# Optimization experiments

Measured on AMD Instinct MI355X. Metric: run time of the kernel, lower is better.

Reference implementation:

```python
import jax, jax.numpy as jnp
import numpy as np

B, D_IN, H, D_OUT = 4096, 4096, 2048, 1000
LN_EPS = 1e-5


def setup_inputs() -> dict:
    key = jax.random.key(0)
    ks = jax.random.split(key, 8)
    s_in = 1.0 / np.sqrt(H)  # torch RNN init: U(-1/sqrt(H), 1/sqrt(H))
    inp = {
        "x": jax.random.normal(ks[0], (B, D_IN), dtype=jnp.float32),
        "W_ih0": jax.random.uniform(ks[1], (H, D_IN), jnp.float32, -s_in, s_in),
        "b_ih0": jax.random.uniform(ks[2], (H,), jnp.float32, -s_in, s_in),
        "b_hh0": jax.random.uniform(ks[3], (H,), jnp.float32, -s_in, s_in),
        "W_ih1": jax.random.uniform(ks[4], (H, H), jnp.float32, -s_in, s_in),
        "b_ih1": jax.random.uniform(ks[5], (H,), jnp.float32, -s_in, s_in),
        "b_hh1": jax.random.uniform(ks[6], (H,), jnp.float32, -s_in, s_in),
        "ln_g": jnp.ones((2 * H,), jnp.float32),
        "ln_b": jnp.zeros((2 * H,), jnp.float32),
        "fc_W": jax.random.uniform(ks[7], (D_OUT, 2 * H), jnp.float32, -1.0 / np.sqrt(2 * H), 1.0 / np.sqrt(2 * H)),
        "fc_b": jnp.zeros((D_OUT,), jnp.float32),
    }
    return inp


def reference(x, W_ih0, b_ih0, b_hh0, W_ih1, b_ih1, b_hh1, ln_g, ln_b, fc_W, fc_b):
    # seq_len == 1, h0 == 0 -> W_hh terms vanish; only biases remain.
    h1 = jnp.tanh(x @ W_ih0.T + b_ih0 + b_hh0)          # [B, H]
    h2 = jnp.tanh(h1 @ W_ih1.T + b_ih1 + b_hh1)         # [B, H]
    # last_hidden == mean_pooled (single step) -> concat duplicates h2
    combined = jnp.concatenate([h2, h2], axis=1)        # [B, 2H]
    mu = combined.mean(axis=-1, keepdims=True)
    var = combined.var(axis=-1, keepdims=True)
    normed = (combined - mu) * jax.lax.rsqrt(var + LN_EPS) * ln_g + ln_b
    # dropout is identity in eval mode
    return normed @ fc_W.T + fc_b                        # [B, D_OUT]
```

## Files before the change

kernel.cpp:

```cpp
#include <hip/hip_runtime.h>
#include <hip/hip_bf16.h>

typedef __attribute__((ext_vector_type(8))) unsigned short ushort8;
typedef __attribute__((ext_vector_type(8))) __bf16 bf16x8;
typedef __attribute__((ext_vector_type(4))) float f32x4;
typedef __attribute__((ext_vector_type(4))) float floatx4;

__device__ __forceinline__ unsigned short f2bf(float f) {
    unsigned u = __builtin_bit_cast(unsigned, f);
    u += 0x7fffu + ((u >> 16) & 1u);
    return (unsigned short)(u >> 16);
}
__device__ __forceinline__ float bf2f(unsigned short h) {
    unsigned u = ((unsigned)h) << 16;
    return __builtin_bit_cast(float, u);
}

__device__ __forceinline__ void gload_lds16(const void* g, void* l) {
    __builtin_amdgcn_global_load_lds(
        (const __attribute__((address_space(1))) void*)g,
        (__attribute__((address_space(3))) void*)l,
        16, 0, 0);
}

#define BAR()   asm volatile("s_barrier" ::: "memory")
#define VMW0()  asm volatile("s_waitcnt vmcnt(0)" ::: "memory")

__global__ __launch_bounds__(256) void prep_kernel(
        const float* __restrict__ x,   unsigned short* __restrict__ xb,
        const float* __restrict__ W0,  unsigned short* __restrict__ w0b,
        const float* __restrict__ W1,  unsigned short* __restrict__ w1b,
        const float* __restrict__ fcW, const float* __restrict__ lng,
        const float* __restrict__ lnb, const float* __restrict__ fcb,
        unsigned short* __restrict__ weff, float* __restrict__ cc,
        float* __restrict__ wsum) {
    const int b = blockIdx.x;
    const int tid = threadIdx.x;
    __shared__ float red[4], redw[4];

    if (b < 14336) {
        const float* in; unsigned short* out; int i;
        if (b < 8192)       { in = x;  out = xb;  i = b * 256 + tid; }
        else if (b < 12288) { in = W0; out = w0b; i = (b - 8192) * 256 + tid; }
        else                { in = W1; out = w1b; i = (b - 12288) * 256 + tid; }
        floatx4 a = ((const floatx4*)in)[2 * i];
        floatx4 c = ((const floatx4*)in)[2 * i + 1];
        ushort8 o;
#pragma unroll
        for (int j = 0; j < 4; ++j) { o[j] = f2bf(a[j]); o[4 + j] = f2bf(c[j]); }
        ((ushort8*)out)[i] = o;
        return;
    }

    const int o = b - 14336;
    if (o >= 1000) {
        ushort8 z = {0, 0, 0, 0, 0, 0, 0, 0};
        ((ushort8*)(weff + (size_t)o * 2048))[tid] = z;
        if (tid == 0) { cc[o] = 0.f; wsum[o] = 0.f; }
        return;
    }
    const float* wrow = fcW + (size_t)o * 4096;
    int j0 = tid * 8;
    floatx4 wa  = *(const floatx4*)(wrow + j0);
    floatx4 wb  = *(const floatx4*)(wrow + j0 + 4);
    floatx4 wa2 = *(const floatx4*)(wrow + 2048 + j0);
    floatx4 wb2 = *(const floatx4*)(wrow + 2048 + j0 + 4);
    floatx4 ga  = *(const floatx4*)(lng + j0);
    floatx4 gb  = *(const floatx4*)(lng + j0 + 4);
    floatx4 ga2 = *(const floatx4*)(lng + 2048 + j0);
    floatx4 gb2 = *(const floatx4*)(lng + 2048 + j0 + 4);
    floatx4 ba  = *(const floatx4*)(lnb + j0);
    floatx4 bb  = *(const floatx4*)(lnb + j0 + 4);
    floatx4 ba2 = *(const floatx4*)(lnb + 2048 + j0);
    floatx4 bb2 = *(const floatx4*)(lnb + 2048 + j0 + 4);
    ushort8 o8;
    float acc = 0.f, ws = 0.f;
#pragma unroll
    for (int j = 0; j < 4; ++j) {
        o8[j] = f2bf(ga[j] * wa[j] + ga2[j] * wa2[j]);
        acc += ba[j] * wa[j] + ba2[j] * wa2[j];
        ws  += bf2f(o8[j]);
        o8[4 + j] = f2bf(gb[j] * wb[j] + gb2[j] * wb2[j]);
        acc += bb[j] * wb[j] + bb2[j] * wb2[j];
        ws  += bf2f(o8[4 + j]);
    }
    ((ushort8*)(weff + (size_t)o * 2048))[tid] = o8;
#pragma unroll
    for (int d = 32; d; d >>= 1) { acc += __shfl_down(acc, d); ws += __shfl_down(ws, d); }
    if ((tid & 63) == 0) { red[tid >> 6] = acc; redw[tid >> 6] = ws; }
    __syncthreads();
    if (tid == 0) {
        cc[o] = fcb[o] + red[0] + red[1] + red[2] + red[3];
        wsum[o] = redw[0] + redw[1] + redw[2] + redw[3];
    }
}

__global__ __launch_bounds__(256) void ln_stats(const unsigned short* __restrict__ h2,
                                                float2* __restrict__ mur) {
    int row = blockIdx.x, tid = threadIdx.x;
    ushort8 v = ((const ushort8*)(h2 + (size_t)row * 2048))[tid];
    float s = 0.f, s2 = 0.f;
#pragma unroll
    for (int j = 0; j < 8; ++j) { float f = bf2f(v[j]); s += f; s2 += f * f; }
#pragma unroll
    for (int d = 32; d; d >>= 1) { s += __shfl_down(s, d); s2 += __shfl_down(s2, d); }
    __shared__ float rs_[4], rs2_[4];
    if ((tid & 63) == 0) { rs_[tid >> 6] = s; rs2_[tid >> 6] = s2; }
    __syncthreads();
    if (tid == 0) {
        float S = rs_[0] + rs_[1] + rs_[2] + rs_[3];
        float S2 = rs2_[0] + rs2_[1] + rs2_[2] + rs2_[3];
        float mu = S * (1.f / 2048.f);
        float var = S2 * (1.f / 2048.f) - mu * mu;
        mur[row] = make_float2(mu, rsqrtf(var + 1e-5f));
    }
}

template <int EPI, int NJ>
__global__ __launch_bounds__(512, 2) void gemm_rp(const unsigned short* __restrict__ A,
                                                  const unsigned short* __restrict__ B,
                                                  int M, int N, int K,
                                                  const float* __restrict__ bias0,
                                                  const float* __restrict__ bias1,
                                                  void* __restrict__ Cout, int ncols,
                                                  const float2* __restrict__ mur,
                                                  const float* __restrict__ wsum) {
    extern __shared__ char smem[];
    constexpr int BUFSZ = 16384 + NJ * 8192;
    const int tid = threadIdx.x;
    const int lane = tid & 63, wid = tid >> 6;
    const int wm = wid >> 2, wn = wid & 3;
    const int fr = lane & 15, g = lane >> 4;

    const int nwg = gridDim.x * gridDim.y;
    const int fid = blockIdx.y * gridDim.x + blockIdx.x;
    const int cpx = nwg >> 3;
    const int sw = (fid & 7) * cpx + (fid >> 3);
    const int bx = sw % gridDim.x, by = sw / gridDim.x;
    const int row0 = by * 128, col0 = bx * (64 * NJ);

    const int tg = tid >> 3;
    const int tcE = ((tid & 7) ^ (tg & 7)) * 8;

    auto stage = [&](int kt, char* buf) {
#pragma unroll
        for (int r = 0; r < 2; ++r)
            gload_lds16(A + (size_t)(row0 + r * 64 + tg) * K + kt * 64 + tcE,
                        buf + r * 8192 + wid * 1024);
#pragma unroll
        for (int rr = 0; rr < NJ; ++rr)
            gload_lds16(B + (size_t)(col0 + rr * 64 + tg) * K + kt * 64 + tcE,
                        buf + 16384 + rr * 8192 + wid * 1024);
    };

    const int xorv = (fr & 7) << 4;
    auto readFrags = [&](bf16x8 (&fa)[4][2], bf16x8 (&fb)[NJ][2], const char* buf) {
#pragma unroll
        for (int m = 0; m < 4; ++m)
#pragma unroll
            for (int kh = 0; kh < 2; ++kh)
                fa[m][kh] = __builtin_bit_cast(bf16x8, *(const ushort8*)(
                    buf + (wm * 64 + m * 16 + fr) * 128 + ((kh * 64 + g * 16) ^ xorv)));
#pragma unroll
        for (int n = 0; n < NJ; ++n)
#pragma unroll
            for (int kh = 0; kh < 2; ++kh)
                fb[n][kh] = __builtin_bit_cast(bf16x8, *(const ushort8*)(
                    buf + 16384 + (wn * (16 * NJ) + n * 16 + fr) * 128 + ((kh * 64 + g * 16) ^ xorv)));
    };

    f32x4 acc[4][NJ];
#pragma unroll
    for (int i = 0; i < 4; ++i)
#pragma unroll
        for (int j = 0; j < NJ; ++j) acc[i][j] = f32x4{0.f, 0.f, 0.f, 0.f};

    auto domfma = [&](bf16x8 (&fa)[4][2], bf16x8 (&fb)[NJ][2]) {
        __builtin_amdgcn_s_setprio(1);
#pragma unroll
        for (int m = 0; m < 4; ++m)
#pragma unroll
            for (int n = 0; n < NJ; ++n)
#pragma unroll
                for (int kh = 0; kh < 2; ++kh)
                    acc[m][n] = __builtin_amdgcn_mfma_f32_16x16x32_bf16(fa[m][kh], fb[n][kh], acc[m][n], 0, 0, 0);
        __builtin_amdgcn_s_setprio(0);
    };

    bf16x8 aX[4][2], bX[NJ][2], aY[4][2], bY[NJ][2];

    stage(0, smem); stage(1, smem + BUFSZ);
    if constexpr (NJ == 4) { asm volatile("s_waitcnt vmcnt(6)" ::: "memory"); }
    else                   { asm volatile("s_waitcnt vmcnt(4)" ::: "memory"); }
    BAR();
    readFrags(aX, bX, smem);

    const int NT = K >> 6;
    for (int t = 0; t < NT; t += 2) {
        if (t + 2 < NT) {
            stage(t + 2, smem + ((t + 2) % 3) * BUFSZ);
            if constexpr (NJ == 4) { asm volatile("s_waitcnt vmcnt(6)" ::: "memory"); }
            else                   { asm volatile("s_waitcnt vmcnt(4)" ::: "memory"); }
        } else {
            VMW0();
        }
        BAR();
        readFrags(aY, bY, smem + ((t + 1) % 3) * BUFSZ);
        domfma(aX, bX);

        if (t + 2 < NT) {
            if (t + 3 < NT) {
                stage(t + 3, smem + ((t + 3) % 3) * BUFSZ);
                if constexpr (NJ == 4) { asm volatile("s_waitcnt vmcnt(6)" ::: "memory"); }
                else                   { asm volatile("s_waitcnt vmcnt(4)" ::: "memory"); }
            } else {
                VMW0();
            }
            BAR();
            readFrags(aX, bX, smem + ((t + 2) % 3) * BUFSZ);
        }
        domfma(aY, bY);
    }

#pragma unroll
    for (int i = 0; i < 4; ++i) {
        int rbase = row0 + wm * 64 + i * 16 + g * 4;
        if (EPI == 0) {
#pragma unroll
            for (int j = 0; j < NJ; ++j) {
                int col = col0 + wn * (16 * NJ) + j * 16 + fr;
                float bsum = bias0[col] + bias1[col];
                unsigned short* O = (unsigned short*)Cout;
#pragma unroll
                for (int r = 0; r < 4; ++r)
                    O[(size_t)(rbase + r) * N + col] = f2bf(tanhf(acc[i][j][r] + bsum));
            }
        } else {
            float2 mr[4];
#pragma unroll
            for (int r = 0; r < 4; ++r) mr[r] = mur[rbase + r];
#pragma unroll
            for (int j = 0; j < NJ; ++j) {
                int col = col0 + wn * (16 * NJ) + j * 16 + fr;
                if (col < ncols) {
                    float ws = wsum[col];
                    float ccv = bias0[col];
                    float* O = (float*)Cout;
#pragma unroll
                    for (int r = 0; r < 4; ++r)
                        O[(size_t)(rbase + r) * ncols + col] =
                            mr[r].y * (acc[i][j][r] - mr[r].x * ws) + ccv;
                }
            }
        }
    }
}

extern "C" void kernel_launch(void* const* d_in, const int* in_sizes, int n_in,
                              void* d_out, int out_size, void* d_ws, size_t ws_size,
                              hipStream_t stream) {
    const float* x   = (const float*)d_in[0];
    const float* W0  = (const float*)d_in[1];
    const float* bi0 = (const float*)d_in[2];
    const float* bh0 = (const float*)d_in[3];
    const float* W1  = (const float*)d_in[4];
    const float* bi1 = (const float*)d_in[5];
    const float* bh1 = (const float*)d_in[6];
    const float* lng = (const float*)d_in[7];
    const float* lnb = (const float*)d_in[8];
    const float* fcW = (const float*)d_in[9];
    const float* fcb = (const float*)d_in[10];
    float* out = (float*)d_out;

    char* w = (char*)d_ws;
    unsigned short* xb   = (unsigned short*)(w);
    unsigned short* w0b  = (unsigned short*)(w + 33554432ull);
    unsigned short* w1b  = (unsigned short*)(w + 50331648ull);
    unsigned short* h1   = (unsigned short*)(w + 58720256ull);
    unsigned short* h2   = (unsigned short*)(w + 75497472ull);
    unsigned short* weff = (unsigned short*)(w + 92274688ull);
    float* cc            = (float*)(w + 96468992ull);
    float* wsum          = (float*)(w + 96473088ull);
    float2* mur          = (float2*)(w + 96477184ull);

    const int SHM0 = 3 * (16384 + 4 * 8192);
    const int SHM1 = 3 * (16384 + 2 * 8192);
    (void)hipFuncSetAttribute((const void*)gemm_rp<0, 4>,
                              hipFuncAttributeMaxDynamicSharedMemorySize, SHM0);
    (void)hipFuncSetAttribute((const void*)gemm_rp<1, 2>,
                              hipFuncAttributeMaxDynamicSharedMemorySize, SHM1);

    prep_kernel<<<15360, 256, 0, stream>>>(x, xb, W0, w0b, W1, w1b,
                                           fcW, lng, lnb, fcb, weff, cc, wsum);
    gemm_rp<0, 4><<<dim3(8, 32), 512, SHM0, stream>>>(xb, w0b, 4096, 2048, 4096,
                                                      bi0, bh0, h1, 2048, nullptr, nullptr);
    gemm_rp<0, 4><<<dim3(8, 32), 512, SHM0, stream>>>(h1, w1b, 4096, 2048, 2048,
                                                      bi1, bh1, h2, 2048, nullptr, nullptr);
    ln_stats<<<4096, 256, 0, stream>>>(h2, mur);
    gemm_rp<1, 2><<<dim3(8, 32), 512, SHM1, stream>>>(h2, weff, 4096, 1024, 2048,
                                                      cc, nullptr, out, 1000, mur, wsum);
}
```

Baseline: 170.3 us.

## Fuse LayerNorm row statistics into second GEMM epilogue, drop ln_stats kernel

```diff
diff --git a/kernel.cpp b/kernel.cpp
--- a/kernel.cpp
+++ b/kernel.cpp
@@ -95,27 +95,6 @@
     }
 }
 
-__global__ __launch_bounds__(256) void ln_stats(const unsigned short* __restrict__ h2,
-                                                float2* __restrict__ mur) {
-    int row = blockIdx.x, tid = threadIdx.x;
-    ushort8 v = ((const ushort8*)(h2 + (size_t)row * 2048))[tid];
-    float s = 0.f, s2 = 0.f;
-#pragma unroll
-    for (int j = 0; j < 8; ++j) { float f = bf2f(v[j]); s += f; s2 += f * f; }
-#pragma unroll
-    for (int d = 32; d; d >>= 1) { s += __shfl_down(s, d); s2 += __shfl_down(s2, d); }
-    __shared__ float rs_[4], rs2_[4];
-    if ((tid & 63) == 0) { rs_[tid >> 6] = s; rs2_[tid >> 6] = s2; }
-    __syncthreads();
-    if (tid == 0) {
-        float S = rs_[0] + rs_[1] + rs_[2] + rs_[3];
-        float S2 = rs2_[0] + rs2_[1] + rs2_[2] + rs2_[3];
-        float mu = S * (1.f / 2048.f);
-        float var = S2 * (1.f / 2048.f) - mu * mu;
-        mur[row] = make_float2(mu, rsqrtf(var + 1e-5f));
-    }
-}
-
 template <int EPI, int NJ>
 __global__ __launch_bounds__(512, 2) void gemm_rp(const unsigned short* __restrict__ A,
                                                   const unsigned short* __restrict__ B,
@@ -123,7 +102,7 @@
                                                   const float* __restrict__ bias0,
                                                   const float* __restrict__ bias1,
                                                   void* __restrict__ Cout, int ncols,
-                                                  const float2* __restrict__ mur,
+                                                  float2* __restrict__ psum,
                                                   const float* __restrict__ wsum) {
     extern __shared__ char smem[];
     constexpr int BUFSZ = 16384 + NJ * 8192;
@@ -222,23 +201,72 @@
         domfma(aY, bY);
     }
 
-#pragma unroll
-    for (int i = 0; i < 4; ++i) {
-        int rbase = row0 + wm * 64 + i * 16 + g * 4;
-        if (EPI == 0) {
+    if constexpr (EPI == 0 || EPI == 2) {
+        float s1[4][4], s2[4][4];
+        if constexpr (EPI == 2) {
+#pragma unroll
+            for (int i = 0; i < 4; ++i)
+#pragma unroll
+                for (int r = 0; r < 4; ++r) { s1[i][r] = 0.f; s2[i][r] = 0.f; }
+        }
+#pragma unroll
+        for (int i = 0; i < 4; ++i) {
+            int rbase = row0 + wm * 64 + i * 16 + g * 4;
 #pragma unroll
             for (int j = 0; j < NJ; ++j) {
                 int col = col0 + wn * (16 * NJ) + j * 16 + fr;
                 float bsum = bias0[col] + bias1[col];
                 unsigned short* O = (unsigned short*)Cout;
 #pragma unroll
-                for (int r = 0; r < 4; ++r)
-                    O[(size_t)(rbase + r) * N + col] = f2bf(tanhf(acc[i][j][r] + bsum));
-            }
-        } else {
+                for (int r = 0; r < 4; ++r) {
+                    unsigned short us = f2bf(tanhf(acc[i][j][r] + bsum));
+                    O[(size_t)(rbase + r) * N + col] = us;
+                    if constexpr (EPI == 2) {
+                        float vb = bf2f(us);
+                        s1[i][r] += vb; s2[i][r] += vb * vb;
+                    }
+                }
+            }
+        }
+        if constexpr (EPI == 2) {
+            __syncthreads();
+            float2* wsums = (float2*)smem;
+#pragma unroll
+            for (int i = 0; i < 4; ++i)
+#pragma unroll
+                for (int r = 0; r < 4; ++r) {
+                    float a = s1[i][r], b = s2[i][r];
+#pragma unroll
+                    for (int mk = 1; mk < 16; mk <<= 1) {
+                        a += __shfl_xor(a, mk);
+                        b += __shfl_xor(b, mk);
+                    }
+                    if (fr == 0)
+                        wsums[(wm * 64 + i * 16 + g * 4 + r) * 4 + wn] = make_float2(a, b);
+                }
+            __syncthreads();
+            if (tid < 128) {
+                float2 p0 = wsums[tid * 4 + 0], p1 = wsums[tid * 4 + 1];
+                float2 p2 = wsums[tid * 4 + 2], p3 = wsums[tid * 4 + 3];
+                psum[(size_t)(row0 + tid) * 8 + bx] =
+                    make_float2(p0.x + p1.x + p2.x + p3.x, p0.y + p1.y + p2.y + p3.y);
+            }
+        }
+    } else {
+#pragma unroll
+        for (int i = 0; i < 4; ++i) {
+            int rbase = row0 + wm * 64 + i * 16 + g * 4;
             float2 mr[4];
 #pragma unroll
-            for (int r = 0; r < 4; ++r) mr[r] = mur[rbase + r];
+            for (int r = 0; r < 4; ++r) {
+                const floatx4* pp = (const floatx4*)(psum + (size_t)(rbase + r) * 8);
+                floatx4 q0 = pp[0], q1 = pp[1], q2 = pp[2], q3 = pp[3];
+                float S  = (q0[0] + q0[2]) + (q1[0] + q1[2]) + (q2[0] + q2[2]) + (q3[0] + q3[2]);
+                float S2 = (q0[1] + q0[3]) + (q1[1] + q1[3]) + (q2[1] + q2[3]) + (q3[1] + q3[3]);
+                float mu = S * (1.f / 2048.f);
+                float var = S2 * (1.f / 2048.f) - mu * mu;
+                mr[r] = make_float2(mu, rsqrtf(var + 1e-5f));
+            }
 #pragma unroll
             for (int j = 0; j < NJ; ++j) {
                 int col = col0 + wn * (16 * NJ) + j * 16 + fr;
@@ -281,12 +309,14 @@
     unsigned short* weff = (unsigned short*)(w + 92274688ull);
     float* cc            = (float*)(w + 96468992ull);
     float* wsum          = (float*)(w + 96473088ull);
-    float2* mur          = (float2*)(w + 96477184ull);
+    float2* psum         = (float2*)(w + 96477184ull);
 
     const int SHM0 = 3 * (16384 + 4 * 8192);
     const int SHM1 = 3 * (16384 + 2 * 8192);
     (void)hipFuncSetAttribute((const void*)gemm_rp<0, 4>,
                               hipFuncAttributeMaxDynamicSharedMemorySize, SHM0);
+    (void)hipFuncSetAttribute((const void*)gemm_rp<2, 4>,
+                              hipFuncAttributeMaxDynamicSharedMemorySize, SHM0);
     (void)hipFuncSetAttribute((const void*)gemm_rp<1, 2>,
                               hipFuncAttributeMaxDynamicSharedMemorySize, SHM1);
 
@@ -294,9 +324,8 @@
                                            fcW, lng, lnb, fcb, weff, cc, wsum);
     gemm_rp<0, 4><<<dim3(8, 32), 512, SHM0, stream>>>(xb, w0b, 4096, 2048, 4096,
                                                       bi0, bh0, h1, 2048, nullptr, nullptr);
-    gemm_rp<0, 4><<<dim3(8, 32), 512, SHM0, stream>>>(h1, w1b, 4096, 2048, 2048,
-                                                      bi1, bh1, h2, 2048, nullptr, nullptr);
-    ln_stats<<<4096, 256, 0, stream>>>(h2, mur);
+    gemm_rp<2, 4><<<dim3(8, 32), 512, SHM0, stream>>>(h1, w1b, 4096, 2048, 2048,
+                                                      bi1, bh1, h2, 2048, psum, nullptr);
     gemm_rp<1, 2><<<dim3(8, 32), 512, SHM1, stream>>>(h2, weff, 4096, 1024, 2048,
-                                                      cc, nullptr, out, 1000, mur, wsum);
-}
+                                                      cc, nullptr, out, 1000, psum, wsum);
+}
```

New measurement: 172.5 us. About the same (+1.3%).
